# Kernel optimization log

Hardware: AMD Instinct MI355X
Metric: run time of the kernel (lower is better)

## Reference

```python
import jax, jax.numpy as jnp
import numpy as np

B, S, L, F = 32, 48, 64, 256


def setup_inputs() -> dict:
    key = jax.random.key(0)
    ks = jax.random.split(key, 7)
    return {
        "features": jax.random.normal(ks[0], (B, S, L, F), dtype=jnp.float32),
        "src_locs": jax.random.normal(ks[1], (B, L, 2), dtype=jnp.float32),
        "tar_locs": jax.random.normal(ks[2], (B, 2), dtype=jnp.float32),
        "W1": jax.random.normal(ks[3], (F, F), dtype=jnp.float32) * (1.0 / np.sqrt(F)),
        "b1": jax.random.normal(ks[4], (F,), dtype=jnp.float32) * 0.02,
        "W2": jax.random.normal(ks[5], (F, 1), dtype=jnp.float32) * (1.0 / np.sqrt(F)),
        "b2": jax.random.normal(ks[6], (1,), dtype=jnp.float32) * 0.02,
    }


def reference(features, src_locs, tar_locs, W1, b1, W2, b2):
    # features: (B, S, L, F); src_locs: (B, L, 2); tar_locs: (B, 2)
    # MLP score: Linear(F,F) + ReLU + Linear(F,1) + ReLU -> (B, S, L, 1)
    attn = jax.nn.relu(jnp.einsum('bslf,fg->bslg', features, W1) + b1)
    attn = jax.nn.relu(jnp.einsum('bslf,fo->bslo', attn, W2) + b2)  # (B,S,L,1)
    # inverse-distance weights over stations: (B, L)
    dists = jnp.sqrt(jnp.sum((src_locs - tar_locs[:, None, :]) ** 2, axis=-1))
    inv_dists = 1.0 / dists  # (B, L)
    # broadcast to (B, 1, L, 1), softmax over src_length axis (axis=2)
    attn_scores = jax.nn.softmax(attn * inv_dists[:, None, :, None], axis=2)
    # weighted sum over stations -> (B, S, F)
    return jnp.sum(features * attn_scores, axis=2)
```

## Files before the change

### kernel.cpp

```cpp
#include <hip/hip_runtime.h>
#include <hip/hip_fp16.h>
#include <math.h>

typedef _Float16 half8 __attribute__((ext_vector_type(8)));
typedef float floatx4 __attribute__((ext_vector_type(4)));

#define BB 32
#define SS 48
#define LL 64
#define FF 256

__global__ __launch_bounds__(256) void prep_w(const float* __restrict__ W1,
                                              _Float16* __restrict__ whi,
                                              _Float16* __restrict__ wlo) {
    int idx = blockIdx.x * 256 + threadIdx.x;
    int j    = idx & 7;
    int lane = (idx >> 3) & 63;
    int nt   = (idx >> 9) & 15;
    int kt   = idx >> 13;
    int k = kt * 32 + ((lane >> 4) & 3) * 8 + j;
    int n = nt * 16 + (lane & 15);
    float x = W1[k * FF + n];
    _Float16 hi = (_Float16)x;
    _Float16 lo = (_Float16)(x - (float)hi);
    whi[idx] = hi;
    wlo[idx] = lo;
}

__global__ __launch_bounds__(256, 2) void ida_mfma(
    const float* __restrict__ features,
    const float* __restrict__ src_locs,
    const float* __restrict__ tar_locs,
    const _Float16* __restrict__ whi,
    const _Float16* __restrict__ wlo,
    const float* __restrict__ b1,
    const float* __restrict__ W2,
    const float* __restrict__ b2,
    float* __restrict__ out)
{
    __shared__ _Float16 Ahi[8192];
    __shared__ _Float16 Alo[8192];
    __shared__ float SP[LL * 4];
    __shared__ float wbuf[LL];

    const int t    = threadIdx.x;
    const int w    = t >> 6;
    const int lane = t & 63;
    const int quad = lane >> 4;
    const int l16  = lane & 15;
    const int bs   = blockIdx.x;
    const int b    = bs / SS;

    const float* Xg = features + (size_t)bs * (LL * FF);

    floatx4 acc[4][4] = {};

    for (int half = 0; half < 2; ++half) {
        __syncthreads();
        #pragma unroll
        for (int ktl = 0; ktl < 4; ++ktl) {
            int kt  = half * 4 + ktl;
            int row = w * 16 + l16;
            int col = kt * 32 + quad * 8;
            const float4* p = (const float4*)(Xg + row * FF + col);
            float4 x0 = p[0], x1 = p[1];
            float xs[8] = {x0.x, x0.y, x0.z, x0.w, x1.x, x1.y, x1.z, x1.w};
            half8 hi, lo;
            #pragma unroll
            for (int j = 0; j < 8; ++j) {
                _Float16 h = (_Float16)xs[j];
                hi[j] = h;
                lo[j] = (_Float16)(xs[j] - (float)h);
            }
            *((half8*)&Ahi[((w * 4 + ktl) * 64 + lane) * 8]) = hi;
            *((half8*)&Alo[((w * 4 + ktl) * 64 + lane) * 8]) = lo;
        }
        __syncthreads();

        #pragma unroll
        for (int ktl = 0; ktl < 4; ++ktl) {
            int kt = half * 4 + ktl;
            half8 bhi[4], blo[4];
            #pragma unroll
            for (int nt = 0; nt < 4; ++nt) {
                int ntg = w * 4 + nt;
                size_t off = ((size_t)(kt * 16 + ntg) * 64 + lane) * 8;
                bhi[nt] = *((const half8*)(whi + off));
                blo[nt] = *((const half8*)(wlo + off));
            }
            #pragma unroll
            for (int mt = 0; mt < 4; ++mt) {
                half8 ahi = *((half8*)&Ahi[((mt * 4 + ktl) * 64 + lane) * 8]);
                half8 alo = *((half8*)&Alo[((mt * 4 + ktl) * 64 + lane) * 8]);
                #pragma unroll
                for (int nt = 0; nt < 4; ++nt) {
                    acc[mt][nt] = __builtin_amdgcn_mfma_f32_16x16x32_f16(ahi, bhi[nt], acc[mt][nt], 0, 0, 0);
                    acc[mt][nt] = __builtin_amdgcn_mfma_f32_16x16x32_f16(ahi, blo[nt], acc[mt][nt], 0, 0, 0);
                    acc[mt][nt] = __builtin_amdgcn_mfma_f32_16x16x32_f16(alo, bhi[nt], acc[mt][nt], 0, 0, 0);
                }
            }
        }
    }

    float b1v[4], w2v[4];
    #pragma unroll
    for (int nt = 0; nt < 4; ++nt) {
        int n = (w * 4 + nt) * 16 + l16;
        b1v[nt] = b1[n];
        w2v[nt] = W2[n];
    }
    #pragma unroll
    for (int mt = 0; mt < 4; ++mt) {
        #pragma unroll
        for (int r = 0; r < 4; ++r) {
            float p = 0.f;
            #pragma unroll
            for (int nt = 0; nt < 4; ++nt) {
                float h = fmaxf(acc[mt][nt][r] + b1v[nt], 0.f);
                p = fmaf(h, w2v[nt], p);
            }
            p += __shfl_xor(p, 1);
            p += __shfl_xor(p, 2);
            p += __shfl_xor(p, 4);
            p += __shfl_xor(p, 8);
            if (l16 == 0) SP[(mt * 16 + quad * 4 + r) * 4 + w] = p;
        }
    }
    __syncthreads();

    if (t < LL) {
        float s = SP[4 * t] + SP[4 * t + 1] + SP[4 * t + 2] + SP[4 * t + 3] + b2[0];
        float score = fmaxf(s, 0.f);
        float dx = src_locs[(b * LL + t) * 2 + 0] - tar_locs[b * 2 + 0];
        float dy = src_locs[(b * LL + t) * 2 + 1] - tar_locs[b * 2 + 1];
        float inv = 1.0f / sqrtf(dx * dx + dy * dy);
        float logit = score * inv;
        float m = logit;
        #pragma unroll
        for (int o = 32; o > 0; o >>= 1) m = fmaxf(m, __shfl_xor(m, o));
        float e = __expf(logit - m);
        float se = e;
        #pragma unroll
        for (int o = 32; o > 0; o >>= 1) se += __shfl_xor(se, o);
        wbuf[t] = e / se;
    }
    __syncthreads();

    {
        float o = 0.f;
        #pragma unroll 8
        for (int l = 0; l < LL; ++l)
            o = fmaf(Xg[l * FF + t], wbuf[l], o);
        out[bs * FF + t] = o;
    }
}

extern "C" void kernel_launch(void* const* d_in, const int* in_sizes, int n_in,
                              void* d_out, int out_size, void* d_ws, size_t ws_size,
                              hipStream_t stream) {
    const float* features = (const float*)d_in[0];
    const float* src_locs = (const float*)d_in[1];
    const float* tar_locs = (const float*)d_in[2];
    const float* W1       = (const float*)d_in[3];
    const float* b1       = (const float*)d_in[4];
    const float* W2       = (const float*)d_in[5];
    const float* b2       = (const float*)d_in[6];
    float* out = (float*)d_out;

    _Float16* whi = (_Float16*)d_ws;
    _Float16* wlo = whi + FF * FF;

    prep_w<<<dim3(FF * FF / 256), dim3(256), 0, stream>>>(W1, whi, wlo);
    ida_mfma<<<dim3(BB * SS), dim3(256), 0, stream>>>(
        features, src_locs, tar_locs, whi, wlo, b1, W2, b2, out);
}
```

Before: 185.1 us.

## Load A fragments directly from global, drop LDS staging, vectorize weighted sum

Removes the LDS staging of the hi/lo fp16 split of the feature tile. Each wave now loads its A fragments straight from global memory for all four M tiles and splits them in registers. This means every wave re-reads the whole 64x256 tile (4x redundant global/L2 reads) instead of sharing it through LDS. The freed LDS and the barrier removal let the launch bound rise to 3 blocks per CU. The final weighted sum over stations now uses float4 loads, with each wave covering 16 stations, followed by a small LDS reduction.

```diff
diff --git a/kernel.cpp b/kernel.cpp
--- a/kernel.cpp
+++ b/kernel.cpp
@@ -27,7 +27,7 @@
     wlo[idx] = lo;
 }
 
-__global__ __launch_bounds__(256, 2) void ida_mfma(
+__global__ __launch_bounds__(256, 3) void ida_mfma(
     const float* __restrict__ features,
     const float* __restrict__ src_locs,
     const float* __restrict__ tar_locs,
@@ -38,10 +38,9 @@
     const float* __restrict__ b2,
     float* __restrict__ out)
 {
-    __shared__ _Float16 Ahi[8192];
-    __shared__ _Float16 Alo[8192];
     __shared__ float SP[LL * 4];
     __shared__ float wbuf[LL];
+    __shared__ float red[4 * FF];
 
     const int t    = threadIdx.x;
     const int w    = t >> 6;
@@ -55,49 +54,32 @@
 
     floatx4 acc[4][4] = {};
 
-    for (int half = 0; half < 2; ++half) {
-        __syncthreads();
+    #pragma unroll
+    for (int kt = 0; kt < 8; ++kt) {
+        half8 bhi[4], blo[4];
         #pragma unroll
-        for (int ktl = 0; ktl < 4; ++ktl) {
-            int kt  = half * 4 + ktl;
-            int row = w * 16 + l16;
-            int col = kt * 32 + quad * 8;
-            const float4* p = (const float4*)(Xg + row * FF + col);
+        for (int nt = 0; nt < 4; ++nt) {
+            size_t off = ((size_t)(kt * 16 + (w * 4 + nt)) * 64 + lane) * 8;
+            bhi[nt] = *((const half8*)(whi + off));
+            blo[nt] = *((const half8*)(wlo + off));
+        }
+        #pragma unroll
+        for (int mt = 0; mt < 4; ++mt) {
+            const float4* p = (const float4*)(Xg + (mt * 16 + l16) * FF + kt * 32 + quad * 8);
             float4 x0 = p[0], x1 = p[1];
             float xs[8] = {x0.x, x0.y, x0.z, x0.w, x1.x, x1.y, x1.z, x1.w};
-            half8 hi, lo;
+            half8 ahi, alo;
             #pragma unroll
             for (int j = 0; j < 8; ++j) {
                 _Float16 h = (_Float16)xs[j];
-                hi[j] = h;
-                lo[j] = (_Float16)(xs[j] - (float)h);
+                ahi[j] = h;
+                alo[j] = (_Float16)(xs[j] - (float)h);
             }
-            *((half8*)&Ahi[((w * 4 + ktl) * 64 + lane) * 8]) = hi;
-            *((half8*)&Alo[((w * 4 + ktl) * 64 + lane) * 8]) = lo;
-        }
-        __syncthreads();
-
-        #pragma unroll
-        for (int ktl = 0; ktl < 4; ++ktl) {
-            int kt = half * 4 + ktl;
-            half8 bhi[4], blo[4];
             #pragma unroll
             for (int nt = 0; nt < 4; ++nt) {
-                int ntg = w * 4 + nt;
-                size_t off = ((size_t)(kt * 16 + ntg) * 64 + lane) * 8;
-                bhi[nt] = *((const half8*)(whi + off));
-                blo[nt] = *((const half8*)(wlo + off));
-            }
-            #pragma unroll
-            for (int mt = 0; mt < 4; ++mt) {
-                half8 ahi = *((half8*)&Ahi[((mt * 4 + ktl) * 64 + lane) * 8]);
-                half8 alo = *((half8*)&Alo[((mt * 4 + ktl) * 64 + lane) * 8]);
-                #pragma unroll
-                for (int nt = 0; nt < 4; ++nt) {
-                    acc[mt][nt] = __builtin_amdgcn_mfma_f32_16x16x32_f16(ahi, bhi[nt], acc[mt][nt], 0, 0, 0);
-                    acc[mt][nt] = __builtin_amdgcn_mfma_f32_16x16x32_f16(ahi, blo[nt], acc[mt][nt], 0, 0, 0);
-                    acc[mt][nt] = __builtin_amdgcn_mfma_f32_16x16x32_f16(alo, bhi[nt], acc[mt][nt], 0, 0, 0);
-                }
+                acc[mt][nt] = __builtin_amdgcn_mfma_f32_16x16x32_f16(ahi, bhi[nt], acc[mt][nt], 0, 0, 0);
+                acc[mt][nt] = __builtin_amdgcn_mfma_f32_16x16x32_f16(ahi, blo[nt], acc[mt][nt], 0, 0, 0);
+                acc[mt][nt] = __builtin_amdgcn_mfma_f32_16x16x32_f16(alo, bhi[nt], acc[mt][nt], 0, 0, 0);
             }
         }
     }
@@ -147,10 +129,25 @@
     __syncthreads();
 
     {
-        float o = 0.f;
-        #pragma unroll 8
-        for (int l = 0; l < LL; ++l)
-            o = fmaf(Xg[l * FF + t], wbuf[l], o);
+        const float4* Xg4 = (const float4*)Xg;
+        floatx4 o = {0.f, 0.f, 0.f, 0.f};
+        #pragma unroll
+        for (int lr = 0; lr < 16; ++lr) {
+            int l = w * 16 + lr;
+            float wl = wbuf[l];
+            float4 x = Xg4[l * 64 + lane];
+            o[0] = fmaf(x.x, wl, o[0]);
+            o[1] = fmaf(x.y, wl, o[1]);
+            o[2] = fmaf(x.z, wl, o[2]);
+            o[3] = fmaf(x.w, wl, o[3]);
+        }
+        #pragma unroll
+        for (int j = 0; j < 4; ++j)
+            red[w * FF + lane * 4 + j] = o[j];
+    }
+    __syncthreads();
+    {
+        float o = red[0 * FF + t] + red[1 * FF + t] + red[2 * FF + t] + red[3 * FF + t];
         out[bs * FF + t] = o;
     }
 }
```

Measured after the change: 201.2 us. 8.7% more time.
